# Optimization experiments

Measured on AMD Instinct MI355X. Metric: run time of the kernel, lower is better.

The kernel has to match this reference:

```python
import jax, jax.numpy as jnp
import numpy as np

N = 100_000   # nodes
E = 1_280_000 # edges
F_IN = 64
HID = 64

def setup_inputs() -> dict:
    key = jax.random.key(0)
    ks = jax.random.split(key, 5)
    x = jax.random.normal(ks[0], (N, F_IN), dtype=jnp.float32)
    edge_index = jax.random.randint(ks[1], (2, E), 0, N, dtype=jnp.int32)
    edge_weight = jax.random.uniform(ks[2], (E,), dtype=jnp.float32)
    s1 = 1.0 / np.sqrt(F_IN)
    W1 = jax.random.uniform(ks[3], (F_IN, HID), minval=-s1, maxval=s1, dtype=jnp.float32)
    b1 = jnp.zeros((HID,), jnp.float32)
    s2 = 1.0 / np.sqrt(HID)
    W2 = jax.random.uniform(ks[4], (HID, 1), minval=-s2, maxval=s2, dtype=jnp.float32)
    b2 = jnp.zeros((1,), jnp.float32)
    return {"x": x, "edge_index": edge_index, "edge_weight": edge_weight,
            "W1": W1, "b1": b1, "W2": W2, "b2": b2}


def reference(x, edge_index, edge_weight, W1, b1, W2, b2):
    # eval mode: edge dropout and feature dropout are identity.
    # GCNConv with add_self_loops=True: A_hat = A + I, D_hat^-1/2 A_hat D_hat^-1/2.
    row, col = edge_index[0], edge_index[1]
    sl = jnp.arange(N, dtype=row.dtype)
    row = jnp.concatenate([row, sl])
    col = jnp.concatenate([col, sl])
    w = jnp.concatenate([edge_weight, jnp.ones((N,), edge_weight.dtype)])
    # symmetric normalization (shared by both conv layers)
    deg = jax.ops.segment_sum(w, col, num_segments=N)          # [N]
    dinv = jnp.where(deg > 0, jax.lax.rsqrt(deg), 0.0)
    norm = dinv[row] * w * dinv[col]                           # [E+N]

    def gcn(h):  # h: [N, d] already linearly transformed
        msg = h[row] * norm[:, None]                           # gather + scale
        return jax.ops.segment_sum(msg, col, num_segments=N)   # scatter-add

    h = gcn(x @ W1) + b1          # conv1
    h = jax.nn.relu(h)            # relu (dropout = identity in eval)
    out = gcn(h @ W2) + b2        # conv2 -> [N, 1]
    return out
```

## Files before the change

kernel.cpp:

```cpp
#include <hip/hip_runtime.h>
#include <hip/hip_fp16.h>

#define CNT_SHIFT 26
#define DEG_MASK  ((1u << CNT_SHIFT) - 1)
#define DEG_SCALE 1048576.0f
#define CAP 8192
#define GSTRIDE 16

typedef __attribute__((ext_vector_type(8))) short short8;
typedef __attribute__((ext_vector_type(4))) float v4f;

__device__ __forceinline__ unsigned short f_to_h16(float f) {
    return __half_as_ushort(__float2half(f));
}
__device__ __forceinline__ float h16_to_f(unsigned short u) {
    return __half2float(__ushort_as_half(u));
}
__device__ __forceinline__ unsigned short f_to_bf16(float f) {
    unsigned int u = __float_as_uint(f);
    u += 0x7fffu + ((u >> 16) & 1u);
    return (unsigned short)(u >> 16);
}
__device__ __forceinline__ unsigned long long mkrec(int r, int c, float wv) {
    return (unsigned long long)r | ((unsigned long long)(c & 511) << 17)
         | ((unsigned long long)f_to_h16(wv) << 26);
}

__global__ __launch_bounds__(256) void k_scatter_gemm(
        const int4* __restrict__ row4, const int4* __restrict__ col4, const float4* __restrict__ w4,
        const int* __restrict__ row, const int* __restrict__ col, const float* __restrict__ w,
        unsigned* __restrict__ gcur, unsigned long long* __restrict__ binrec,
        const float* __restrict__ x, const float* __restrict__ W1,
        char* __restrict__ h1q, float* __restrict__ scales,
        int E4, int rem, int nBlkE, int nGemm, int n, int nbkt) {
    __shared__ int h[256];
    int blk = blockIdx.x, t = threadIdx.x;
    if (blk < nBlkE) {
        h[t] = 0;
        __syncthreads();
        int base = blk * 1024;
#pragma unroll
        for (int k = 0; k < 4; ++k) {
            int g = base + k * 256 + t;
            if (g < E4) {
                int4 c = col4[g];
                atomicAdd(&h[c.x >> 9], 1);
                atomicAdd(&h[c.y >> 9], 1);
                atomicAdd(&h[c.z >> 9], 1);
                atomicAdd(&h[c.w >> 9], 1);
            }
        }
        if (blk == 0 && t < rem) atomicAdd(&h[col[4 * E4 + t] >> 9], 1);
        __syncthreads();
        if (t < nbkt) {
            int bb = t + (blk % nbkt);
            bb -= (bb >= nbkt) ? nbkt : 0;
            int cnt = h[bb];
            int runbase = 0;
            if (cnt > 0) runbase = (int)atomicAdd(&gcur[(size_t)bb * GSTRIDE], (unsigned)cnt);
            h[bb] = bb * CAP + runbase;
        }
        __syncthreads();
#pragma unroll
        for (int k = 0; k < 4; ++k) {
            int g = base + k * 256 + t;
            if (g < E4) {
                int4   r = row4[g];
                int4   c = col4[g];
                float4 v = w4[g];
                { int pos = atomicAdd(&h[c.x >> 9], 1); binrec[pos] = mkrec(r.x, c.x, v.x); }
                { int pos = atomicAdd(&h[c.y >> 9], 1); binrec[pos] = mkrec(r.y, c.y, v.y); }
                { int pos = atomicAdd(&h[c.z >> 9], 1); binrec[pos] = mkrec(r.z, c.z, v.z); }
                { int pos = atomicAdd(&h[c.w >> 9], 1); binrec[pos] = mkrec(r.w, c.w, v.w); }
            }
        }
        if (blk == 0 && t < rem) {
            int e = 4 * E4 + t;
            int c = col[e];
            int pos = atomicAdd(&h[c >> 9], 1);
            binrec[pos] = mkrec(row[e], c, w[e]);
        }
    } else {
        int b = blk - nBlkE;
        int lane = t & 63;
        int wave = t >> 6;
        int q   = lane >> 4;
        int n16 = lane & 15;
        short8 bf[8];
#pragma unroll
        for (int ct = 0; ct < 4; ++ct) {
#pragma unroll
            for (int hh = 0; hh < 2; ++hh) {
                short8 v;
#pragma unroll
                for (int j = 0; j < 8; ++j)
                    v[j] = (short)f_to_bf16(W1[(hh * 32 + q * 8 + j) * 64 + ct * 16 + n16]);
                bf[ct * 2 + hh] = v;
            }
        }
        int ntile = (n + 15) >> 4;
        int stride = nGemm * 4;
        for (int tile = b * 4 + wave; tile < ntile; tile += stride) {
            int base = tile << 4;
            short8 a0, a1;
            if (base + 16 <= n) {
                const float* xr = x + (size_t)(base + n16) * 64 + q * 8;
                float4 u0 = *(const float4*)(xr);
                float4 u1 = *(const float4*)(xr + 4);
                float4 u2 = *(const float4*)(xr + 32);
                float4 u3 = *(const float4*)(xr + 36);
                a0[0] = (short)f_to_bf16(u0.x); a0[1] = (short)f_to_bf16(u0.y);
                a0[2] = (short)f_to_bf16(u0.z); a0[3] = (short)f_to_bf16(u0.w);
                a0[4] = (short)f_to_bf16(u1.x); a0[5] = (short)f_to_bf16(u1.y);
                a0[6] = (short)f_to_bf16(u1.z); a0[7] = (short)f_to_bf16(u1.w);
                a1[0] = (short)f_to_bf16(u2.x); a1[1] = (short)f_to_bf16(u2.y);
                a1[2] = (short)f_to_bf16(u2.z); a1[3] = (short)f_to_bf16(u2.w);
                a1[4] = (short)f_to_bf16(u3.x); a1[5] = (short)f_to_bf16(u3.y);
                a1[6] = (short)f_to_bf16(u3.z); a1[7] = (short)f_to_bf16(u3.w);
            } else {
                bool ok = (base + n16) < n;
                const float* xr = x + (size_t)(ok ? (base + n16) : 0) * 64 + q * 8;
#pragma unroll
                for (int j = 0; j < 8; ++j) {
                    a0[j] = ok ? (short)f_to_bf16(xr[j])      : (short)0;
                    a1[j] = ok ? (short)f_to_bf16(xr[32 + j]) : (short)0;
                }
            }
            v4f acc0 = {0.f, 0.f, 0.f, 0.f}, acc1 = acc0, acc2 = acc0, acc3 = acc0;
            acc0 = __builtin_amdgcn_mfma_f32_16x16x32_bf16(a0, bf[0], acc0, 0, 0, 0);
            acc0 = __builtin_amdgcn_mfma_f32_16x16x32_bf16(a1, bf[1], acc0, 0, 0, 0);
            acc1 = __builtin_amdgcn_mfma_f32_16x16x32_bf16(a0, bf[2], acc1, 0, 0, 0);
            acc1 = __builtin_amdgcn_mfma_f32_16x16x32_bf16(a1, bf[3], acc1, 0, 0, 0);
            acc2 = __builtin_amdgcn_mfma_f32_16x16x32_bf16(a0, bf[4], acc2, 0, 0, 0);
            acc2 = __builtin_amdgcn_mfma_f32_16x16x32_bf16(a1, bf[5], acc2, 0, 0, 0);
            acc3 = __builtin_amdgcn_mfma_f32_16x16x32_bf16(a0, bf[6], acc3, 0, 0, 0);
            acc3 = __builtin_amdgcn_mfma_f32_16x16x32_bf16(a1, bf[7], acc3, 0, 0, 0);
#pragma unroll
            for (int r = 0; r < 4; ++r) {
                int rowg = base + q * 4 + r;
                if (rowg >= n) break;
                float m = fmaxf(fmaxf(fabsf(acc0[r]), fabsf(acc1[r])),
                                fmaxf(fabsf(acc2[r]), fabsf(acc3[r])));
                m = fmaxf(m, __shfl_xor(m, 1, 64));
                m = fmaxf(m, __shfl_xor(m, 2, 64));
                m = fmaxf(m, __shfl_xor(m, 4, 64));
                m = fmaxf(m, __shfl_xor(m, 8, 64));
                m = fmaxf(m, 1e-20f);
                float inv = 127.0f / m;
                unsigned char* dst = (unsigned char*)h1q + (size_t)rowg * 64 + n16;
                dst[0]  = (unsigned char)(__float2int_rn(acc0[r] * inv) + 128);
                dst[16] = (unsigned char)(__float2int_rn(acc1[r] * inv) + 128);
                dst[32] = (unsigned char)(__float2int_rn(acc2[r] * inv) + 128);
                dst[48] = (unsigned char)(__float2int_rn(acc3[r] * inv) + 128);
                if (n16 == 0) scales[rowg] = m * (1.0f / 127.0f);
            }
        }
    }
}

__global__ __launch_bounds__(256) void k_bucket(
        const unsigned long long* __restrict__ binrec, const unsigned* __restrict__ gcur,
        float* __restrict__ dinv, int* __restrict__ off, int* __restrict__ bktend,
        unsigned* __restrict__ ep, float* __restrict__ scales,
        int N, int nbkt) {
    __shared__ unsigned cnt[512];
    __shared__ int   loff[512];
    __shared__ int   ssum[256];
    int b = blockIdx.x, t = threadIdx.x;
    int e0 = b * CAP;
    int tot = (int)gcur[(size_t)b * GSTRIDE];
    int e1 = e0 + tot;
    cnt[t] = 0u; cnt[t + 256] = 0u;
    __syncthreads();
    unsigned epw[32];
    unsigned crk[32];
#pragma unroll
    for (int k = 0; k < 32; ++k) {
        int i = e0 + t + k * 256;
        if (i < e1) {
            unsigned long long rec = binrec[i];
            int cl = (int)((rec >> 17) & 511);
            unsigned hb = (unsigned)((rec >> 26) & 0xFFFF);
            float wv = h16_to_f((unsigned short)hb);
            unsigned old = atomicAdd(&cnt[cl],
                                     (1u << CNT_SHIFT) + (unsigned)(wv * DEG_SCALE + 0.5f));
            unsigned rank = old >> CNT_SHIFT;
            epw[k] = ((unsigned)(rec & 0x1FFFF) << 15) | (hb & 0x7fffu);
            crk[k] = ((unsigned)cl << 16) | rank;
        }
    }
    __syncthreads();
    unsigned p0 = cnt[2 * t], p1 = cnt[2 * t + 1];
    int c0 = (int)(p0 >> CNT_SHIFT), c1 = (int)(p1 >> CNT_SHIFT);
    float d0 = rsqrtf((float)(p0 & DEG_MASK) * (1.0f / DEG_SCALE) + 1.0f);
    float d1 = rsqrtf((float)(p1 & DEG_MASK) * (1.0f / DEG_SCALE) + 1.0f);
    int ps = c0 + c1;
    ssum[t] = ps;
    __syncthreads();
    for (int o = 1; o < 256; o <<= 1) {
        int v = (t >= o) ? ssum[t - o] : 0;
        __syncthreads();
        ssum[t] += v;
        __syncthreads();
    }
    int excl = ssum[t] - ps;
    loff[2 * t] = excl;
    loff[2 * t + 1] = excl + c0;
    int id0 = (b << 9) + 2 * t, id1 = id0 + 1;
    if (id0 < N) { dinv[id0] = d0; scales[id0] *= d0; off[id0] = e0 + excl; }
    if (id1 < N) { dinv[id1] = d1; scales[id1] *= d1; off[id1] = e0 + excl + c0; }
    if (t == 0) bktend[b] = e1;
    __syncthreads();
#pragma unroll
    for (int k = 0; k < 32; ++k) {
        int i = e0 + t + k * 256;
        if (i < e1) {
            int cl   = (int)(crk[k] >> 16);
            int rank = (int)(crk[k] & 0xFFFFu);
            ep[e0 + loff[cl] + rank] = epw[k];
        }
    }
}

__global__ __launch_bounds__(256) void k_agg1(
        const char* __restrict__ h1q_, const float* __restrict__ scales,
        const int* __restrict__ off, const int* __restrict__ bktend,
        const unsigned* __restrict__ ep,
        const float* __restrict__ dinv, const float* __restrict__ b1,
        const float* __restrict__ W2,
        float* __restrict__ h2, int n) {
    const unsigned char* __restrict__ h1q = (const unsigned char*)h1q_;
    __shared__ uint2 tbl[4][64];
    int lane = threadIdx.x & 63;
    int wave = threadIdx.x >> 6;
    int grp  = lane >> 4;
    int fl   = (lane & 15) * 4;
    int i = blockIdx.x * 4 + wave;
    if (i >= n) return;
    float di = dinv[i];
    int s  = off[i];
    int s1 = (((i & 511) == 511) || (i == n - 1)) ? bktend[i >> 9] : off[i + 1];

    float4 acc;
    float S;
    {
        unsigned q4 = *(const unsigned*)(h1q + (size_t)i * 64 + fl);
        float si = (grp == 0) ? scales[i] : 0.f;
        acc.x = (float)(q4 & 0xffu)         * si;
        acc.y = (float)((q4 >> 8) & 0xffu)  * si;
        acc.z = (float)((q4 >> 16) & 0xffu) * si;
        acc.w = (float)(q4 >> 24)           * si;
        S = si;
    }
    for (int c0 = s; c0 < s1; c0 += 64) {
        int cl = s1 - c0; if (cl > 64) cl = 64;
        {
            unsigned src = 0u; float m = 0.f;
            if (lane < cl) {
                unsigned e = ep[c0 + lane];
                src = e >> 15;
                m = scales[src] * h16_to_f((unsigned short)(e & 0x7fff));
            }
            tbl[wave][lane] = make_uint2(src, __float_as_uint(m));
        }
        for (int j0 = 0; j0 < cl; j0 += 8) {
            uint2 ta = tbl[wave][j0 + grp];
            uint2 tb = tbl[wave][j0 + 4 + grp];
            float ma = __uint_as_float(ta.y);
            float mb = __uint_as_float(tb.y);
            unsigned qa = *(const unsigned*)(h1q + ((size_t)ta.x << 6) + fl);
            unsigned qb = *(const unsigned*)(h1q + ((size_t)tb.x << 6) + fl);
            acc.x = fmaf((float)(qa & 0xffu),         ma, acc.x);
            acc.y = fmaf((float)((qa >> 8) & 0xffu),  ma, acc.y);
            acc.z = fmaf((float)((qa >> 16) & 0xffu), ma, acc.z);
            acc.w = fmaf((float)(qa >> 24),           ma, acc.w);
            acc.x = fmaf((float)(qb & 0xffu),         mb, acc.x);
            acc.y = fmaf((float)((qb >> 8) & 0xffu),  mb, acc.y);
            acc.z = fmaf((float)((qb >> 16) & 0xffu), mb, acc.z);
            acc.w = fmaf((float)(qb >> 24),           mb, acc.w);
            S += ma + mb;
        }
    }
    acc.x += __shfl_xor(acc.x, 16, 64); acc.x += __shfl_xor(acc.x, 32, 64);
    acc.y += __shfl_xor(acc.y, 16, 64); acc.y += __shfl_xor(acc.y, 32, 64);
    acc.z += __shfl_xor(acc.z, 16, 64); acc.z += __shfl_xor(acc.z, 32, 64);
    acc.w += __shfl_xor(acc.w, 16, 64); acc.w += __shfl_xor(acc.w, 32, 64);
    S += __shfl_xor(S, 16, 64); S += __shfl_xor(S, 32, 64);
    acc.x = fmaf(S, -128.f, acc.x);
    acc.y = fmaf(S, -128.f, acc.y);
    acc.z = fmaf(S, -128.f, acc.z);
    acc.w = fmaf(S, -128.f, acc.w);
    float4 bb = *(const float4*)(b1 + fl);
    float4 ww = *(const float4*)(W2 + fl);
    float p = fmaxf(fmaf(di, acc.x, bb.x), 0.f) * ww.x
            + fmaxf(fmaf(di, acc.y, bb.y), 0.f) * ww.y
            + fmaxf(fmaf(di, acc.z, bb.z), 0.f) * ww.z
            + fmaxf(fmaf(di, acc.w, bb.w), 0.f) * ww.w;
#pragma unroll
    for (int o = 1; o < 16; o <<= 1) p += __shfl_xor(p, o, 64);
    if (lane == 0) h2[i] = di * p;
}

__global__ void k_agg2(const float* __restrict__ h2,
                       const int* __restrict__ off, const int* __restrict__ bktend,
                       const unsigned* __restrict__ ep, const float* __restrict__ dinv,
                       const float* __restrict__ b2, float* __restrict__ out, int n) {
    int i = blockIdx.x * 256 + threadIdx.x;
    if (i >= n) return;
    float acc = h2[i];
    int s = off[i];
    int s1 = (((i & 511) == 511) || (i == n - 1)) ? bktend[i >> 9] : off[i + 1];
    for (; s + 8 <= s1; s += 8) {
        unsigned e0 = ep[s],     e1 = ep[s + 1], e2 = ep[s + 2], e3 = ep[s + 3];
        unsigned e4 = ep[s + 4], e5 = ep[s + 5], e6 = ep[s + 6], e7 = ep[s + 7];
        float v0 = h2[e0 >> 15], v1 = h2[e1 >> 15], v2 = h2[e2 >> 15], v3 = h2[e3 >> 15];
        float v4 = h2[e4 >> 15], v5 = h2[e5 >> 15], v6 = h2[e6 >> 15], v7 = h2[e7 >> 15];
        acc = fmaf(v0, h16_to_f((unsigned short)(e0 & 0x7fff)), acc);
        acc = fmaf(v1, h16_to_f((unsigned short)(e1 & 0x7fff)), acc);
        acc = fmaf(v2, h16_to_f((unsigned short)(e2 & 0x7fff)), acc);
        acc = fmaf(v3, h16_to_f((unsigned short)(e3 & 0x7fff)), acc);
        acc = fmaf(v4, h16_to_f((unsigned short)(e4 & 0x7fff)), acc);
        acc = fmaf(v5, h16_to_f((unsigned short)(e5 & 0x7fff)), acc);
        acc = fmaf(v6, h16_to_f((unsigned short)(e6 & 0x7fff)), acc);
        acc = fmaf(v7, h16_to_f((unsigned short)(e7 & 0x7fff)), acc);
    }
    for (; s + 4 <= s1; s += 4) {
        unsigned e0 = ep[s], e1 = ep[s + 1], e2 = ep[s + 2], e3 = ep[s + 3];
        float v0 = h2[e0 >> 15], v1 = h2[e1 >> 15], v2 = h2[e2 >> 15], v3 = h2[e3 >> 15];
        acc = fmaf(v0, h16_to_f((unsigned short)(e0 & 0x7fff)), acc);
        acc = fmaf(v1, h16_to_f((unsigned short)(e1 & 0x7fff)), acc);
        acc = fmaf(v2, h16_to_f((unsigned short)(e2 & 0x7fff)), acc);
        acc = fmaf(v3, h16_to_f((unsigned short)(e3 & 0x7fff)), acc);
    }
    for (; s < s1; ++s) {
        unsigned e = ep[s];
        acc = fmaf(h2[e >> 15], h16_to_f((unsigned short)(e & 0x7fff)), acc);
    }
    out[i] = dinv[i] * acc + b2[0];
}

extern "C" void kernel_launch(void* const* d_in, const int* in_sizes, int n_in,
                              void* d_out, int out_size, void* d_ws, size_t ws_size,
                              hipStream_t stream) {
    const float* x  = (const float*)d_in[0];
    const int*   ei = (const int*)d_in[1];
    const float* w  = (const float*)d_in[2];
    const float* W1 = (const float*)d_in[3];
    const float* b1 = (const float*)d_in[4];
    const float* W2 = (const float*)d_in[5];
    const float* b2 = (const float*)d_in[6];
    float* out = (float*)d_out;

    const int N = in_sizes[0] / 64;
    const int E = in_sizes[2];
    const int* row = ei;
    const int* col = ei + E;

    const int nbkt  = (N + 511) >> 9;
    const int E4    = E / 4;
    const int rem   = E - 4 * E4;
    const int nBlkE = (E4 + 1023) / 1024;
    const int nGemm = 1024;

    char* p = (char*)d_ws;
    auto take = [&](size_t bytes) { char* q = p; p += (bytes + 15) & ~(size_t)15; return q; };
    unsigned long long* binrec = (unsigned long long*)take((size_t)nbkt * CAP * 8);
    unsigned* gcur = (unsigned*)take((size_t)nbkt * GSTRIDE * 4);
    int* bktend  = (int*)take((size_t)nbkt * 4);
    char* h1q    = (char*)take((size_t)N * 64);
    float* scales= (float*)take((size_t)N * 4);
    float* dinv  = (float*)take((size_t)N * 4);
    int*   off   = (int*)take((size_t)(N + 1) * 4);
    unsigned* ep = (unsigned*)take((size_t)nbkt * CAP * 4);
    float* h2    = (float*)take((size_t)N * 4);

    (void)hipMemsetAsync(gcur, 0, (size_t)nbkt * GSTRIDE * 4, stream);
    k_scatter_gemm<<<nBlkE + nGemm, 256, 0, stream>>>(
        (const int4*)row, (const int4*)col, (const float4*)w,
        row, col, w, gcur, binrec, x, W1, h1q, scales,
        E4, rem, nBlkE, nGemm, N, nbkt);
    k_bucket<<<nbkt, 256, 0, stream>>>(binrec, gcur, dinv, off, bktend, ep, scales, N, nbkt);
    k_agg1<<<(N + 3) / 4, 256, 0, stream>>>(h1q, scales, off, bktend, ep, dinv, b1, W2, h2, N);
    k_agg2<<<(N + 255) / 256, 256, 0, stream>>>(h2, off, bktend, ep, dinv, b2, out, N);
}
```

Before: 174.8 us.

## Assign one node per 16-lane group in first aggregation kernel

The first aggregation kernel now has each 16-lane group own one node, so a wave handles four nodes instead of splitting one node's edges across four groups. This removes the cross-group shuffle reduction and cuts the launched block count by four. The gather loop is unrolled to four loads per iteration. In exchange, all four groups in a wave iterate to the largest degree among their nodes, which wastes lanes on divergent degree counts and makes each lane's chain of dependent gathers longer.

```diff
diff --git a/kernel.cpp b/kernel.cpp
--- a/kernel.cpp
+++ b/kernel.cpp
@@ -230,62 +230,74 @@
         const float* __restrict__ W2,
         float* __restrict__ h2, int n) {
     const unsigned char* __restrict__ h1q = (const unsigned char*)h1q_;
-    __shared__ uint2 tbl[4][64];
-    int lane = threadIdx.x & 63;
-    int wave = threadIdx.x >> 6;
-    int grp  = lane >> 4;
-    int fl   = (lane & 15) * 4;
-    int i = blockIdx.x * 4 + wave;
-    if (i >= n) return;
-    float di = dinv[i];
-    int s  = off[i];
-    int s1 = (((i & 511) == 511) || (i == n - 1)) ? bktend[i >> 9] : off[i + 1];
-
-    float4 acc;
-    float S;
-    {
-        unsigned q4 = *(const unsigned*)(h1q + (size_t)i * 64 + fl);
-        float si = (grp == 0) ? scales[i] : 0.f;
+    __shared__ uint2 tbl[4][4][65];
+    int t = threadIdx.x;
+    int lane = t & 63, wave = t >> 6, grp = lane >> 4, f15 = lane & 15, fl = f15 * 4;
+    int i = blockIdx.x * 16 + wave * 4 + grp;
+    bool alive = i < n;
+    int s = 0, s1 = 0;
+    if (alive) {
+        s = off[i];
+        s1 = (((i & 511) == 511) || (i == n - 1)) ? bktend[i >> 9] : off[i + 1];
+    }
+    int deg = s1 - s;
+    int md = max(deg, __shfl_xor(deg, 16, 64));
+    md = max(md, __shfl_xor(md, 32, 64));
+    float di = alive ? dinv[i] : 0.f;
+    float4 acc = {0.f, 0.f, 0.f, 0.f};
+    float S = 0.f;
+    if (alive) {
+        unsigned q4 = *(const unsigned*)(h1q + ((size_t)i << 6) + fl);
+        float si = scales[i];
         acc.x = (float)(q4 & 0xffu)         * si;
         acc.y = (float)((q4 >> 8) & 0xffu)  * si;
         acc.z = (float)((q4 >> 16) & 0xffu) * si;
         acc.w = (float)(q4 >> 24)           * si;
         S = si;
     }
-    for (int c0 = s; c0 < s1; c0 += 64) {
-        int cl = s1 - c0; if (cl > 64) cl = 64;
-        {
+    for (int c0 = 0; c0 < md; c0 += 64) {
+        int remg = deg - c0;
+        int mrem = md - c0; if (mrem > 64) mrem = 64;
+        for (int k = 0; k * 16 < mrem; ++k) {
+            int slot = k * 16 + f15;
             unsigned src = 0u; float m = 0.f;
-            if (lane < cl) {
-                unsigned e = ep[c0 + lane];
+            if (slot < remg) {
+                unsigned e = ep[s + c0 + slot];
                 src = e >> 15;
-                m = scales[src] * h16_to_f((unsigned short)(e & 0x7fff));
-            }
-            tbl[wave][lane] = make_uint2(src, __float_as_uint(m));
-        }
-        for (int j0 = 0; j0 < cl; j0 += 8) {
-            uint2 ta = tbl[wave][j0 + grp];
-            uint2 tb = tbl[wave][j0 + 4 + grp];
-            float ma = __uint_as_float(ta.y);
-            float mb = __uint_as_float(tb.y);
-            unsigned qa = *(const unsigned*)(h1q + ((size_t)ta.x << 6) + fl);
-            unsigned qb = *(const unsigned*)(h1q + ((size_t)tb.x << 6) + fl);
-            acc.x = fmaf((float)(qa & 0xffu),         ma, acc.x);
-            acc.y = fmaf((float)((qa >> 8) & 0xffu),  ma, acc.y);
-            acc.z = fmaf((float)((qa >> 16) & 0xffu), ma, acc.z);
-            acc.w = fmaf((float)(qa >> 24),           ma, acc.w);
-            acc.x = fmaf((float)(qb & 0xffu),         mb, acc.x);
-            acc.y = fmaf((float)((qb >> 8) & 0xffu),  mb, acc.y);
-            acc.z = fmaf((float)((qb >> 16) & 0xffu), mb, acc.z);
-            acc.w = fmaf((float)(qb >> 24),           mb, acc.w);
-            S += ma + mb;
-        }
-    }
-    acc.x += __shfl_xor(acc.x, 16, 64); acc.x += __shfl_xor(acc.x, 32, 64);
-    acc.y += __shfl_xor(acc.y, 16, 64); acc.y += __shfl_xor(acc.y, 32, 64);
-    acc.z += __shfl_xor(acc.z, 16, 64); acc.z += __shfl_xor(acc.z, 32, 64);
-    acc.w += __shfl_xor(acc.w, 16, 64); acc.w += __shfl_xor(acc.w, 32, 64);
-    S += __shfl_xor(S, 16, 64); S += __shfl_xor(S, 32, 64);
+                m = scales[src] * h16_to_f((unsigned short)(e & 0x7fffu));
+            }
+            tbl[wave][grp][slot] = make_uint2(src, __float_as_uint(m));
+        }
+        for (int j = 0; j < mrem; j += 4) {
+            uint2 t0 = tbl[wave][grp][j];
+            uint2 t1 = tbl[wave][grp][j + 1];
+            uint2 t2 = tbl[wave][grp][j + 2];
+            uint2 t3 = tbl[wave][grp][j + 3];
+            unsigned q0 = *(const unsigned*)(h1q + ((size_t)t0.x << 6) + fl);
+            unsigned q1 = *(const unsigned*)(h1q + ((size_t)t1.x << 6) + fl);
+            unsigned q2 = *(const unsigned*)(h1q + ((size_t)t2.x << 6) + fl);
+            unsigned q3 = *(const unsigned*)(h1q + ((size_t)t3.x << 6) + fl);
+            float m0 = __uint_as_float(t0.y), m1 = __uint_as_float(t1.y);
+            float m2 = __uint_as_float(t2.y), m3 = __uint_as_float(t3.y);
+            acc.x = fmaf((float)(q0 & 0xffu),         m0, acc.x);
+            acc.y = fmaf((float)((q0 >> 8) & 0xffu),  m0, acc.y);
+            acc.z = fmaf((float)((q0 >> 16) & 0xffu), m0, acc.z);
+            acc.w = fmaf((float)(q0 >> 24),           m0, acc.w);
+            acc.x = fmaf((float)(q1 & 0xffu),         m1, acc.x);
+            acc.y = fmaf((float)((q1 >> 8) & 0xffu),  m1, acc.y);
+            acc.z = fmaf((float)((q1 >> 16) & 0xffu), m1, acc.z);
+            acc.w = fmaf((float)(q1 >> 24),           m1, acc.w);
+            acc.x = fmaf((float)(q2 & 0xffu),         m2, acc.x);
+            acc.y = fmaf((float)((q2 >> 8) & 0xffu),  m2, acc.y);
+            acc.z = fmaf((float)((q2 >> 16) & 0xffu), m2, acc.z);
+            acc.w = fmaf((float)(q2 >> 24),           m2, acc.w);
+            acc.x = fmaf((float)(q3 & 0xffu),         m3, acc.x);
+            acc.y = fmaf((float)((q3 >> 8) & 0xffu),  m3, acc.y);
+            acc.z = fmaf((float)((q3 >> 16) & 0xffu), m3, acc.z);
+            acc.w = fmaf((float)(q3 >> 24),           m3, acc.w);
+            S += (m0 + m1) + (m2 + m3);
+        }
+    }
     acc.x = fmaf(S, -128.f, acc.x);
     acc.y = fmaf(S, -128.f, acc.y);
     acc.z = fmaf(S, -128.f, acc.z);
@@ -298,7 +310,7 @@
             + fmaxf(fmaf(di, acc.w, bb.w), 0.f) * ww.w;
 #pragma unroll
     for (int o = 1; o < 16; o <<= 1) p += __shfl_xor(p, o, 64);
-    if (lane == 0) h2[i] = di * p;
+    if (f15 == 0 && alive) h2[i] = di * p;
 }
 
 __global__ void k_agg2(const float* __restrict__ h2,
@@ -380,6 +392,6 @@
         row, col, w, gcur, binrec, x, W1, h1q, scales,
         E4, rem, nBlkE, nGemm, N, nbkt);
     k_bucket<<<nbkt, 256, 0, stream>>>(binrec, gcur, dinv, off, bktend, ep, scales, N, nbkt);
-    k_agg1<<<(N + 3) / 4, 256, 0, stream>>>(h1q, scales, off, bktend, ep, dinv, b1, W2, h2, N);
+    k_agg1<<<(N + 15) / 16, 256, 0, stream>>>(h1q, scales, off, bktend, ep, dinv, b1, W2, h2, N);
     k_agg2<<<(N + 255) / 256, 256, 0, stream>>>(h2, off, bktend, ep, dinv, b2, out, N);
 }
```

Measured after the change: 161.6 us. 1.08x faster.
